# Kernel tuning notes

Measured on AMD Instinct MI355X. Metric: run time of the kernel, lower is better.

Reference implementation:

```python
import jax, jax.numpy as jnp
import numpy as np

B, T, A, H = 64, 512, 128, 512  # batch, timesteps, alphabet, hidden (m_size == H)


def setup_inputs() -> dict:
    key = jax.random.key(0)
    ks = jax.random.split(key, 8)
    s_ih = 1.0 / np.sqrt(H)
    return {
        "inputs": jax.random.normal(ks[0], (B, T, A), dtype=jnp.float32),
        # PyTorch LSTMCell params: gate order i, f, g, o
        "w_ih": jax.random.uniform(ks[1], (4 * H, A), jnp.float32, -s_ih, s_ih),
        "w_hh": jax.random.uniform(ks[2], (4 * H, H), jnp.float32, -s_ih, s_ih),
        "b_ih": jax.random.uniform(ks[3], (4 * H,), jnp.float32, -s_ih, s_ih),
        "b_hh": jax.random.uniform(ks[4], (4 * H,), jnp.float32, -s_ih, s_ih),
        # per-sample fast-weight matrix M (initialized to zeros in the module,
        # but trainable; use small random values so the bmm path is exercised)
        "M": jax.random.normal(ks[5], (B, H, H), dtype=jnp.float32) * 0.02,
        # hidden2out Linear
        "w_out": jax.random.uniform(ks[6], (A, H), jnp.float32, -s_ih, s_ih),
        "b_out": jax.random.uniform(ks[7], (A,), jnp.float32, -s_ih, s_ih),
        "h0": jnp.zeros((B, H), jnp.float32),
        "c0": jnp.zeros((B, H), jnp.float32),
    }


def reference(inputs, w_ih, w_hh, b_ih, b_hh, M, w_out, b_out, h0, c0):
    bias = b_ih + b_hh

    def step(carry, x_t):
        h, c = carry
        gates = x_t @ w_ih.T + h @ w_hh.T + bias  # [B, 4H]
        i, f, g, o = jnp.split(gates, 4, axis=1)
        i = jax.nn.sigmoid(i)
        f = jax.nn.sigmoid(f)
        g = jnp.tanh(g)
        o = jax.nn.sigmoid(o)
        c_new = f * c + i * g
        h_new = o * jnp.tanh(c_new)
        # fast-weight augmentation: h + M @ h (m_size == hidden_dim branch)
        h_aug = h_new + jnp.einsum('bij,bj->bi', M, h_new)
        out = h_aug @ w_out.T + b_out  # [B, A]
        # use_aug_in_recurrent=False: recurrent state stays un-augmented
        return (h_new, c_new), out

    xs = jnp.swapaxes(inputs, 0, 1)  # [T, B, A]
    _, outs = jax.lax.scan(step, (h0, c0), xs)  # outs: [T, B, A]
    return jnp.swapaxes(outs, 0, 1)  # [B, T, A]
```

## Files before the change

### kernel.cpp

```cpp
#include <hip/hip_runtime.h>
#include <hip/hip_bf16.h>

#define T_STEPS 512
#define B_SZ    64
#define A_SZ    128
#define H_SZ    512
#define NWG     256
#define THR     512

#define WEFF_SZ 4194304u
#define HBUF_SZ 65536u
#define BAR_U32 512u

#define W_F4    8192
#define ACT_F4  1280
#define LDSB    (4*(W_F4 + ACT_F4)*4 + 256)

__global__ __launch_bounds__(256) void weff_kernel(
    const float* __restrict__ M, const float* __restrict__ w_out,
    float* __restrict__ weff)
{
    __shared__ float wl[32*36];
    __shared__ float ml[32*68];
    const int blk = blockIdx.x;
    const int b   = blk >> 5;
    const int at  = (blk >> 3) & 3;
    const int jt  = blk & 7;
    const int tid = threadIdx.x;
    const int ap  = tid >> 4;
    const int jq  = tid & 15;
    float4 acc0 = {0.f,0.f,0.f,0.f};
    float4 acc1 = {0.f,0.f,0.f,0.f};

    for (int ik = 0; ik < 16; ++ik){
        {
            const int a = tid >> 3, i4 = tid & 7;
            const float4 v = *(const float4*)&w_out[(at*32 + a)*512 + ik*32 + i4*4];
            *(float4*)&wl[a*36 + i4*4] = v;
        }
        {
            const int i = tid >> 3, j8 = tid & 7;
            const float* src = &M[((size_t)b*512 + (size_t)(ik*32 + i))*512 + jt*64 + j8*8];
            const float4 v0 = *(const float4*)(src);
            const float4 v1 = *(const float4*)(src + 4);
            *(float4*)&ml[i*68 + j8*8]     = v0;
            *(float4*)&ml[i*68 + j8*8 + 4] = v1;
        }
        __syncthreads();
        #pragma unroll
        for (int i0 = 0; i0 < 32; i0 += 4){
            const float4 w0 = *(const float4*)&wl[(ap*2+0)*36 + i0];
            const float4 w1 = *(const float4*)&wl[(ap*2+1)*36 + i0];
            #pragma unroll
            for (int di = 0; di < 4; ++di){
                const float4 mv = *(const float4*)&ml[(i0+di)*68 + jq*4];
                const float wa = (di==0)?w0.x:(di==1)?w0.y:(di==2)?w0.z:w0.w;
                const float wb = (di==0)?w1.x:(di==1)?w1.y:(di==2)?w1.z:w1.w;
                acc0.x = fmaf(wa, mv.x, acc0.x); acc0.y = fmaf(wa, mv.y, acc0.y);
                acc0.z = fmaf(wa, mv.z, acc0.z); acc0.w = fmaf(wa, mv.w, acc0.w);
                acc1.x = fmaf(wb, mv.x, acc1.x); acc1.y = fmaf(wb, mv.y, acc1.y);
                acc1.z = fmaf(wb, mv.z, acc1.z); acc1.w = fmaf(wb, mv.w, acc1.w);
            }
        }
        __syncthreads();
    }
    const int ag = at*32 + ap*2;
    const int jg = jt*64 + jq*4;
    {
        const float4 id0 = *(const float4*)&w_out[(ag+0)*512 + jg];
        const float4 id1 = *(const float4*)&w_out[(ag+1)*512 + jg];
        float4 o0, o1;
        o0.x = acc0.x + id0.x; o0.y = acc0.y + id0.y; o0.z = acc0.z + id0.z; o0.w = acc0.w + id0.w;
        o1.x = acc1.x + id1.x; o1.y = acc1.y + id1.y; o1.z = acc1.z + id1.z; o1.w = acc1.w + id1.w;
        *(float4*)&weff[((size_t)b*128 + (ag+0))*512 + jg] = o0;
        *(float4*)&weff[((size_t)b*128 + (ag+1))*512 + jg] = o1;
    }
}

__global__ __launch_bounds__(THR) void rnn_kernel(
    const float* __restrict__ x,    const float* __restrict__ w_ih,
    const float* __restrict__ w_hh, const float* __restrict__ b_ih,
    const float* __restrict__ b_hh, const float* __restrict__ h0,
    const float* __restrict__ c0,   const float* __restrict__ b_out,
    const float* __restrict__ weff, float* __restrict__ hbuf,
    unsigned* __restrict__ barws,   float* __restrict__ out)
{
    extern __shared__ float lds[];
    float4* wlds4  = (float4*)lds;
    float4* act4   = ((float4*)lds) + W_F4;
    float*  bias_s = lds + 4*(W_F4 + ACT_F4);
    __shared__ unsigned role_s;

    const int tid = threadIdx.x;

    if (tid == 0){
        unsigned xcc;
        asm volatile("s_getreg_b32 %0, hwreg(20, 0, 32)" : "=s"(xcc));
        xcc &= 7u;
        const unsigned slot = __hip_atomic_fetch_add(&barws[xcc*64 + 2], 1u,
                                  __ATOMIC_RELAXED, __HIP_MEMORY_SCOPE_AGENT);
        role_s = (xcc << 5) | (slot & 31u);
    }
    __syncthreads();
    const int myx = (int)(role_s >> 5);
    const int s   = (int)(role_s & 31u);
    const int b0  = myx * 8;
    const int j0  = s * 16;

    unsigned* cnt = &barws[myx*64 + 0];
    unsigned* gen = &barws[myx*64 + 1];
    float* hbX = hbuf + myx * 8192;

    {
        const int r = tid >> 3, p = tid & 7;
        const int g = r & 3, jlr = r >> 2;
        const float4* src = (const float4*)&w_hh[(size_t)(g*H_SZ + j0 + jlr)*H_SZ];
        const int e = r & 7;
        #pragma unroll
        for (int m = 0; m < 16; ++m){
            const int sl = p*16 + m;
            wlds4[r*128 + (sl ^ e)] = src[sl];
        }
    }
    if (tid < 64){
        const int g = tid & 3, jlr = tid >> 2;
        const int grow = g*H_SZ + j0 + jlr;
        bias_s[tid] = b_ih[grow] + b_hh[grow];
    }

    const int jl  = tid >> 5;
    const int ks  = tid & 31;
    const int sb  = tid >> 6;
    const int l   = tid & 63;
    const int c_l = (tid >> 4) & 3;
    const int k_l = tid & 15;
    const int col = s*4 + c_l;
    const int eb  = sb & 7;

    float4 wihv[4];
    #pragma unroll
    for (int g = 0; g < 4; ++g)
        wihv[g] = *(const float4*)&w_ih[(size_t)(g*H_SZ + j0 + jl)*A_SZ + ks*4];

    float4 wef4[8];
    #pragma unroll
    for (int i8 = 0; i8 < 8; ++i8)
        wef4[i8] = *(const float4*)&weff[((size_t)(b0 + sb)*A_SZ + col)*H_SZ + (k_l + 16*i8)*4];
    const float bo = b_out[col];

    float cst[8];
    #pragma unroll
    for (int bb = 0; bb < 8; ++bb)
        cst[bb] = c0[(size_t)(b0 + bb)*H_SZ + j0 + jl];

    for (int t = 0; t <= T_STEPS; ++t){
        {
            const float* hprev = hbX + (((t+1)&1) ? 4096 : 0) + sb*H_SZ;
            const float4* h0r  = (const float4*)&h0[(size_t)(b0+sb)*H_SZ];
            const float4* xr   = (const float4*)&x[((size_t)(b0+sb)*T_STEPS + (t < T_STEPS ? t : 0))*A_SZ];
            auto stage_one = [&](int sl){
                float4 v;
                if (sl < 32){
                    if (t < T_STEPS){ v = xr[sl]; act4[sb*160 + (sl ^ eb)] = v; }
                } else if (t == 0){
                    v = h0r[sl - 32];
                    act4[sb*160 + (sl ^ eb)] = v;
                } else {
                    float* hp = (float*)(hprev + (sl - 32)*4);
                    v.x = __hip_atomic_load(hp+0, __ATOMIC_RELAXED, __HIP_MEMORY_SCOPE_AGENT);
                    v.y = __hip_atomic_load(hp+1, __ATOMIC_RELAXED, __HIP_MEMORY_SCOPE_AGENT);
                    v.z = __hip_atomic_load(hp+2, __ATOMIC_RELAXED, __HIP_MEMORY_SCOPE_AGENT);
                    v.w = __hip_atomic_load(hp+3, __ATOMIC_RELAXED, __HIP_MEMORY_SCOPE_AGENT);
                    act4[sb*160 + (sl ^ eb)] = v;
                }
            };
            stage_one(2*l);
            stage_one(2*l + 1);
            if (l < 32) stage_one(128 + l);
        }
        __syncthreads();

        if (t > 0){
            float p = 0.f;
            #pragma unroll
            for (int i8 = 0; i8 < 8; ++i8){
                const float4 av = act4[sb*160 + ((32 + k_l + 16*i8) ^ eb)];
                p = fmaf(wef4[i8].x, av.x, p);
                p = fmaf(wef4[i8].y, av.y, p);
                p = fmaf(wef4[i8].z, av.z, p);
                p = fmaf(wef4[i8].w, av.w, p);
            }
            p += __shfl_xor(p, 1); p += __shfl_xor(p, 2);
            p += __shfl_xor(p, 4); p += __shfl_xor(p, 8);
            if (k_l == 0)
                out[((size_t)(b0 + sb)*T_STEPS + (t-1))*A_SZ + col] = p + bo;
        }
        if (t == T_STEPS) break;

        float acc[4][8];
        #pragma unroll
        for (int g = 0; g < 4; ++g)
            #pragma unroll
            for (int bb = 0; bb < 8; ++bb) acc[g][bb] = 0.f;

        {
            float4 av[8];
            #pragma unroll
            for (int bb = 0; bb < 8; ++bb) av[bb] = act4[bb*160 + (ks ^ (bb&7))];
            #pragma unroll
            for (int g = 0; g < 4; ++g){
                #pragma unroll
                for (int bb = 0; bb < 8; ++bb){
                    acc[g][bb] = fmaf(wihv[g].x, av[bb].x, acc[g][bb]);
                    acc[g][bb] = fmaf(wihv[g].y, av[bb].y, acc[g][bb]);
                    acc[g][bb] = fmaf(wihv[g].z, av[bb].z, acc[g][bb]);
                    acc[g][bb] = fmaf(wihv[g].w, av[bb].w, acc[g][bb]);
                }
            }
        }
        #pragma unroll
        for (int m = 0; m < 4; ++m){
            const int hs = ks + 32*m;
            float4 wv[4];
            #pragma unroll
            for (int g = 0; g < 4; ++g){
                const int r = jl*4 + g;
                wv[g] = wlds4[r*128 + (hs ^ (r&7))];
            }
            float4 av[8];
            #pragma unroll
            for (int bb = 0; bb < 8; ++bb) av[bb] = act4[bb*160 + ((32 + hs) ^ (bb&7))];
            #pragma unroll
            for (int g = 0; g < 4; ++g)
                #pragma unroll
                for (int bb = 0; bb < 8; ++bb){
                    acc[g][bb] = fmaf(wv[g].x, av[bb].x, acc[g][bb]);
                    acc[g][bb] = fmaf(wv[g].y, av[bb].y, acc[g][bb]);
                    acc[g][bb] = fmaf(wv[g].z, av[bb].z, acc[g][bb]);
                    acc[g][bb] = fmaf(wv[g].w, av[bb].w, acc[g][bb]);
                }
        }
        #pragma unroll
        for (int g = 0; g < 4; ++g)
            #pragma unroll
            for (int bb = 0; bb < 8; ++bb){
                float v = acc[g][bb];
                v += __shfl_xor(v, 1);  v += __shfl_xor(v, 2);
                v += __shfl_xor(v, 4);  v += __shfl_xor(v, 8);
                v += __shfl_xor(v, 16);
                acc[g][bb] = v;
            }

        if (ks == 0){
            float* hc = hbX + ((t&1) ? 4096 : 0);
            #pragma unroll
            for (int bb = 0; bb < 8; ++bb){
                const float gi = acc[0][bb] + bias_s[jl*4 + 0];
                const float gf = acc[1][bb] + bias_s[jl*4 + 1];
                const float gg = acc[2][bb] + bias_s[jl*4 + 2];
                const float go = acc[3][bb] + bias_s[jl*4 + 3];
                const float si = 1.f / (1.f + __expf(-gi));
                const float sf = 1.f / (1.f + __expf(-gf));
                const float tg = tanhf(gg);
                const float so = 1.f / (1.f + __expf(-go));
                const float c  = sf * cst[bb] + si * tg;
                cst[bb] = c;
                const float h  = so * tanhf(c);
                __hip_atomic_store(&hc[bb*H_SZ + j0 + jl], h,
                                   __ATOMIC_RELAXED, __HIP_MEMORY_SCOPE_AGENT);
            }
        }
        __syncthreads();

        if (tid == 0){
            __atomic_signal_fence(__ATOMIC_SEQ_CST);
            const unsigned prev = __hip_atomic_fetch_add(cnt, 1u,
                                      __ATOMIC_RELAXED, __HIP_MEMORY_SCOPE_AGENT);
            if (prev + 1u == 32u*(unsigned)(t+1)){
                __hip_atomic_store(gen, (unsigned)(t+1),
                                   __ATOMIC_RELAXED, __HIP_MEMORY_SCOPE_AGENT);
            } else {
                while (__hip_atomic_load(gen, __ATOMIC_RELAXED,
                                         __HIP_MEMORY_SCOPE_AGENT) < (unsigned)(t+1))
                    __builtin_amdgcn_s_sleep(2);
            }
            __atomic_signal_fence(__ATOMIC_SEQ_CST);
        }
        __syncthreads();
    }
}

extern "C" void kernel_launch(void* const* d_in, const int* in_sizes, int n_in,
                              void* d_out, int out_size, void* d_ws, size_t ws_size,
                              hipStream_t stream)
{
    (void)in_sizes; (void)n_in; (void)out_size;
    const float* x     = (const float*)d_in[0];
    const float* w_ih  = (const float*)d_in[1];
    const float* w_hh  = (const float*)d_in[2];
    const float* b_ih  = (const float*)d_in[3];
    const float* b_hh  = (const float*)d_in[4];
    const float* M     = (const float*)d_in[5];
    const float* w_out = (const float*)d_in[6];
    const float* b_out = (const float*)d_in[7];
    const float* h0    = (const float*)d_in[8];
    const float* c0    = (const float*)d_in[9];
    float* out = (float*)d_out;

    const size_t need = (size_t)(WEFF_SZ + HBUF_SZ)*4 + BAR_U32*4;
    if (ws_size < need) return;

    float*    ws    = (float*)d_ws;
    float*    weff  = ws;
    float*    hbuf  = ws + WEFF_SZ;
    unsigned* barws = (unsigned*)(ws + WEFF_SZ + HBUF_SZ);

    hipMemsetAsync((void*)barws, 0, BAR_U32*4, stream);

    hipLaunchKernelGGL(weff_kernel, dim3(2048), dim3(256), 0, stream, M, w_out, weff);

    hipFuncSetAttribute((const void*)rnn_kernel,
                        hipFuncAttributeMaxDynamicSharedMemorySize, LDSB);

    void* args[] = {
        (void*)&x, (void*)&w_ih, (void*)&w_hh, (void*)&b_ih, (void*)&b_hh,
        (void*)&h0, (void*)&c0, (void*)&b_out, (void*)&weff, (void*)&hbuf,
        (void*)&barws, (void*)&out
    };
    hipLaunchCooperativeKernel((const void*)rnn_kernel, dim3(NWG), dim3(THR),
                               args, (unsigned)LDSB, stream);
}
```

Baseline: 12.90 ms.

## Replace counter barrier with per-block flags, register-resident weights, DPP reductions

```diff
diff --git a/kernel.cpp b/kernel.cpp
--- a/kernel.cpp
+++ b/kernel.cpp
@@ -10,11 +10,8 @@
 
 #define WEFF_SZ 4194304u
 #define HBUF_SZ 65536u
-#define BAR_U32 512u
-
-#define W_F4    8192
-#define ACT_F4  1280
-#define LDSB    (4*(W_F4 + ACT_F4)*4 + 256)
+#define BAR_U32 2048u
+#define LDSB    98304
 
 __global__ __launch_bounds__(256) void weff_kernel(
     const float* __restrict__ M, const float* __restrict__ w_out,
@@ -77,7 +74,29 @@
     }
 }
 
-__global__ __launch_bounds__(THR) void rnn_kernel(
+template<int CTRL>
+__device__ __forceinline__ float dppadd(float v){
+    const int o = __builtin_amdgcn_mov_dpp(__float_as_int(v), CTRL, 0xF, 0xF, true);
+    return v + __int_as_float(o);
+}
+__device__ __forceinline__ float red16(float v){
+    v = dppadd<0xB1>(v); v = dppadd<0x4E>(v);
+    v = dppadd<0x141>(v); v = dppadd<0x140>(v);
+    return v;
+}
+__device__ __forceinline__ float red32(float v){
+    v = red16(v);
+    v += __int_as_float(__builtin_amdgcn_ds_swizzle(__float_as_int(v), 0x401F));
+    return v;
+}
+__device__ __forceinline__ float sigm(float x){ return 1.f / (1.f + __expf(-x)); }
+__device__ __forceinline__ float tanh_fast(float x){
+    const float xc = fminf(fmaxf(x, -9.f), 9.f);
+    const float e  = __expf(2.f * xc);
+    return (e - 1.f) * (1.f / (e + 1.f));
+}
+
+__global__ __launch_bounds__(THR, 2) void rnn_kernel(
     const float* __restrict__ x,    const float* __restrict__ w_ih,
     const float* __restrict__ w_hh, const float* __restrict__ b_ih,
     const float* __restrict__ b_hh, const float* __restrict__ h0,
@@ -86,9 +105,7 @@
     unsigned* __restrict__ barws,   float* __restrict__ out)
 {
     extern __shared__ float lds[];
-    float4* wlds4  = (float4*)lds;
-    float4* act4   = ((float4*)lds) + W_F4;
-    float*  bias_s = lds + 4*(W_F4 + ACT_F4);
+    float4* act = (float4*)lds;
     __shared__ unsigned role_s;
 
     const int tid = threadIdx.x;
@@ -97,7 +114,7 @@
         unsigned xcc;
         asm volatile("s_getreg_b32 %0, hwreg(20, 0, 32)" : "=s"(xcc));
         xcc &= 7u;
-        const unsigned slot = __hip_atomic_fetch_add(&barws[xcc*64 + 2], 1u,
+        const unsigned slot = __hip_atomic_fetch_add(&barws[xcc*256 + 0], 1u,
                                   __ATOMIC_RELAXED, __HIP_MEMORY_SCOPE_AGENT);
         role_s = (xcc << 5) | (slot & 31u);
     }
@@ -107,26 +124,8 @@
     const int b0  = myx * 8;
     const int j0  = s * 16;
 
-    unsigned* cnt = &barws[myx*64 + 0];
-    unsigned* gen = &barws[myx*64 + 1];
-    float* hbX = hbuf + myx * 8192;
-
-    {
-        const int r = tid >> 3, p = tid & 7;
-        const int g = r & 3, jlr = r >> 2;
-        const float4* src = (const float4*)&w_hh[(size_t)(g*H_SZ + j0 + jlr)*H_SZ];
-        const int e = r & 7;
-        #pragma unroll
-        for (int m = 0; m < 16; ++m){
-            const int sl = p*16 + m;
-            wlds4[r*128 + (sl ^ e)] = src[sl];
-        }
-    }
-    if (tid < 64){
-        const int g = tid & 3, jlr = tid >> 2;
-        const int grow = g*H_SZ + j0 + jlr;
-        bias_s[tid] = b_ih[grow] + b_hh[grow];
-    }
+    unsigned* flg  = barws + myx*256 + 32;
+    float*    hbX  = hbuf + myx * 8192;
 
     const int jl  = tid >> 5;
     const int ks  = tid & 31;
@@ -135,158 +134,158 @@
     const int c_l = (tid >> 4) & 3;
     const int k_l = tid & 15;
     const int col = s*4 + c_l;
-    const int eb  = sb & 7;
-
+
+    float4 whh[4][4];
+    #pragma unroll
+    for (int g = 0; g < 4; ++g)
+        #pragma unroll
+        for (int m = 0; m < 4; ++m)
+            whh[g][m] = *(const float4*)&w_hh[(size_t)(g*H_SZ + j0 + jl)*H_SZ + (ks + 32*m)*4];
     float4 wihv[4];
     #pragma unroll
     for (int g = 0; g < 4; ++g)
         wihv[g] = *(const float4*)&w_ih[(size_t)(g*H_SZ + j0 + jl)*A_SZ + ks*4];
-
+    float bg[4];
+    #pragma unroll
+    for (int g = 0; g < 4; ++g){
+        const int grow = g*H_SZ + j0 + jl;
+        bg[g] = b_ih[grow] + b_hh[grow];
+    }
     float4 wef4[8];
     #pragma unroll
     for (int i8 = 0; i8 < 8; ++i8)
         wef4[i8] = *(const float4*)&weff[((size_t)(b0 + sb)*A_SZ + col)*H_SZ + (k_l + 16*i8)*4];
     const float bo = b_out[col];
-
-    float cst[8];
+    float cst = c0[(size_t)(b0 + (ks & 7))*H_SZ + j0 + jl];
+
+    float4 xv[8];
     #pragma unroll
     for (int bb = 0; bb < 8; ++bb)
-        cst[bb] = c0[(size_t)(b0 + bb)*H_SZ + j0 + jl];
+        xv[bb] = *(const float4*)&x[((size_t)(b0+bb)*T_STEPS + 0)*A_SZ + ks*4];
 
     for (int t = 0; t <= T_STEPS; ++t){
         {
-            const float* hprev = hbX + (((t+1)&1) ? 4096 : 0) + sb*H_SZ;
-            const float4* h0r  = (const float4*)&h0[(size_t)(b0+sb)*H_SZ];
-            const float4* xr   = (const float4*)&x[((size_t)(b0+sb)*T_STEPS + (t < T_STEPS ? t : 0))*A_SZ];
-            auto stage_one = [&](int sl){
-                float4 v;
-                if (sl < 32){
-                    if (t < T_STEPS){ v = xr[sl]; act4[sb*160 + (sl ^ eb)] = v; }
-                } else if (t == 0){
-                    v = h0r[sl - 32];
-                    act4[sb*160 + (sl ^ eb)] = v;
-                } else {
-                    float* hp = (float*)(hprev + (sl - 32)*4);
-                    v.x = __hip_atomic_load(hp+0, __ATOMIC_RELAXED, __HIP_MEMORY_SCOPE_AGENT);
-                    v.y = __hip_atomic_load(hp+1, __ATOMIC_RELAXED, __HIP_MEMORY_SCOPE_AGENT);
-                    v.z = __hip_atomic_load(hp+2, __ATOMIC_RELAXED, __HIP_MEMORY_SCOPE_AGENT);
-                    v.w = __hip_atomic_load(hp+3, __ATOMIC_RELAXED, __HIP_MEMORY_SCOPE_AGENT);
-                    act4[sb*160 + (sl ^ eb)] = v;
+            const int bb = sb;
+            if (t > 0){
+                unsigned* f1 = flg + ((l >> 2)       ) * 4;
+                unsigned* f2 = flg + (16 + (l >> 2)  ) * 4;
+                while (__hip_atomic_load(f1, __ATOMIC_RELAXED, __HIP_MEMORY_SCOPE_AGENT)
+                       < (unsigned)t) __builtin_amdgcn_s_sleep(1);
+                while (__hip_atomic_load(f2, __ATOMIC_RELAXED, __HIP_MEMORY_SCOPE_AGENT)
+                       < (unsigned)t) __builtin_amdgcn_s_sleep(1);
+            }
+            const float4* hb = (t == 0)
+                ? ((const float4*)h0)  + (size_t)(b0 + bb)*128
+                : ((const float4*)hbX) + (((t+1)&1) ? 1024 : 0) + bb*128;
+            const float4* p1 = hb + l;
+            const float4* p2 = hb + l + 64;
+            float4 v1, v2;
+            asm volatile("global_load_dwordx4 %0, %2, off sc0\n\t"
+                         "global_load_dwordx4 %1, %3, off sc0\n\t"
+                         "s_waitcnt vmcnt(0)"
+                         : "=&v"(v1), "=&v"(v2) : "v"(p1), "v"(p2) : "memory");
+            act[bb*128 + l]      = v1;
+            act[bb*128 + l + 64] = v2;
+        }
+        __syncthreads();
+
+        if (t < T_STEPS){
+            float acc[4][8];
+            #pragma unroll
+            for (int g = 0; g < 4; ++g)
+                #pragma unroll
+                for (int bb = 0; bb < 8; ++bb) acc[g][bb] = 0.f;
+
+            #pragma unroll
+            for (int bb = 0; bb < 8; ++bb){
+                const float4 av = xv[bb];
+                #pragma unroll
+                for (int g = 0; g < 4; ++g){
+                    acc[g][bb] = fmaf(wihv[g].x, av.x, acc[g][bb]);
+                    acc[g][bb] = fmaf(wihv[g].y, av.y, acc[g][bb]);
+                    acc[g][bb] = fmaf(wihv[g].z, av.z, acc[g][bb]);
+                    acc[g][bb] = fmaf(wihv[g].w, av.w, acc[g][bb]);
                 }
-            };
-            stage_one(2*l);
-            stage_one(2*l + 1);
-            if (l < 32) stage_one(128 + l);
-        }
-        __syncthreads();
+            }
+            #pragma unroll
+            for (int m = 0; m < 4; ++m){
+                float4 av[8];
+                #pragma unroll
+                for (int bb = 0; bb < 8; ++bb) av[bb] = act[bb*128 + ks + 32*m];
+                #pragma unroll
+                for (int g = 0; g < 4; ++g){
+                    const float4 wv = whh[g][m];
+                    #pragma unroll
+                    for (int bb = 0; bb < 8; ++bb){
+                        acc[g][bb] = fmaf(wv.x, av[bb].x, acc[g][bb]);
+                        acc[g][bb] = fmaf(wv.y, av[bb].y, acc[g][bb]);
+                        acc[g][bb] = fmaf(wv.z, av[bb].z, acc[g][bb]);
+                        acc[g][bb] = fmaf(wv.w, av[bb].w, acc[g][bb]);
+                    }
+                }
+            }
+            #pragma unroll
+            for (int g = 0; g < 4; ++g)
+                #pragma unroll
+                for (int bb = 0; bb < 8; ++bb)
+                    acc[g][bb] = red32(acc[g][bb]);
+
+            float ga[4];
+            const bool q0 = ks & 1, q1 = ks & 2, q2 = ks & 4;
+            #pragma unroll
+            for (int g = 0; g < 4; ++g){
+                const float a01 = q0 ? acc[g][1] : acc[g][0];
+                const float a23 = q0 ? acc[g][3] : acc[g][2];
+                const float a45 = q0 ? acc[g][5] : acc[g][4];
+                const float a67 = q0 ? acc[g][7] : acc[g][6];
+                const float a03 = q1 ? a23 : a01;
+                const float a47 = q1 ? a67 : a45;
+                ga[g] = q2 ? a47 : a03;
+            }
+            if (ks < 8){
+                const float gi = ga[0] + bg[0];
+                const float gf = ga[1] + bg[1];
+                const float gg = ga[2] + bg[2];
+                const float go = ga[3] + bg[3];
+                const float si = sigm(gi);
+                const float sf = sigm(gf);
+                const float tg = tanh_fast(gg);
+                const float so = sigm(go);
+                const float c  = sf * cst + si * tg;
+                cst = c;
+                const float h  = so * tanh_fast(c);
+                float* hw = hbX + ((t&1) ? 4096 : 0);
+                hw[(size_t)ks*H_SZ + j0 + jl] = h;
+            }
+        }
 
         if (t > 0){
             float p = 0.f;
             #pragma unroll
             for (int i8 = 0; i8 < 8; ++i8){
-                const float4 av = act4[sb*160 + ((32 + k_l + 16*i8) ^ eb)];
+                const float4 av = act[sb*128 + k_l + 16*i8];
                 p = fmaf(wef4[i8].x, av.x, p);
                 p = fmaf(wef4[i8].y, av.y, p);
                 p = fmaf(wef4[i8].z, av.z, p);
                 p = fmaf(wef4[i8].w, av.w, p);
             }
-            p += __shfl_xor(p, 1); p += __shfl_xor(p, 2);
-            p += __shfl_xor(p, 4); p += __shfl_xor(p, 8);
+            p = red16(p);
             if (k_l == 0)
                 out[((size_t)(b0 + sb)*T_STEPS + (t-1))*A_SZ + col] = p + bo;
         }
         if (t == T_STEPS) break;
 
-        float acc[4][8];
-        #pragma unroll
-        for (int g = 0; g < 4; ++g)
-            #pragma unroll
-            for (int bb = 0; bb < 8; ++bb) acc[g][bb] = 0.f;
-
-        {
-            float4 av[8];
-            #pragma unroll
-            for (int bb = 0; bb < 8; ++bb) av[bb] = act4[bb*160 + (ks ^ (bb&7))];
-            #pragma unroll
-            for (int g = 0; g < 4; ++g){
-                #pragma unroll
-                for (int bb = 0; bb < 8; ++bb){
-                    acc[g][bb] = fmaf(wihv[g].x, av[bb].x, acc[g][bb]);
-                    acc[g][bb] = fmaf(wihv[g].y, av[bb].y, acc[g][bb]);
-                    acc[g][bb] = fmaf(wihv[g].z, av[bb].z, acc[g][bb]);
-                    acc[g][bb] = fmaf(wihv[g].w, av[bb].w, acc[g][bb]);
-                }
-            }
-        }
-        #pragma unroll
-        for (int m = 0; m < 4; ++m){
-            const int hs = ks + 32*m;
-            float4 wv[4];
-            #pragma unroll
-            for (int g = 0; g < 4; ++g){
-                const int r = jl*4 + g;
-                wv[g] = wlds4[r*128 + (hs ^ (r&7))];
-            }
-            float4 av[8];
-            #pragma unroll
-            for (int bb = 0; bb < 8; ++bb) av[bb] = act4[bb*160 + ((32 + hs) ^ (bb&7))];
-            #pragma unroll
-            for (int g = 0; g < 4; ++g)
-                #pragma unroll
-                for (int bb = 0; bb < 8; ++bb){
-                    acc[g][bb] = fmaf(wv[g].x, av[bb].x, acc[g][bb]);
-                    acc[g][bb] = fmaf(wv[g].y, av[bb].y, acc[g][bb]);
-                    acc[g][bb] = fmaf(wv[g].z, av[bb].z, acc[g][bb]);
-                    acc[g][bb] = fmaf(wv[g].w, av[bb].w, acc[g][bb]);
-                }
-        }
-        #pragma unroll
-        for (int g = 0; g < 4; ++g)
-            #pragma unroll
-            for (int bb = 0; bb < 8; ++bb){
-                float v = acc[g][bb];
-                v += __shfl_xor(v, 1);  v += __shfl_xor(v, 2);
-                v += __shfl_xor(v, 4);  v += __shfl_xor(v, 8);
-                v += __shfl_xor(v, 16);
-                acc[g][bb] = v;
-            }
-
-        if (ks == 0){
-            float* hc = hbX + ((t&1) ? 4096 : 0);
-            #pragma unroll
-            for (int bb = 0; bb < 8; ++bb){
-                const float gi = acc[0][bb] + bias_s[jl*4 + 0];
-                const float gf = acc[1][bb] + bias_s[jl*4 + 1];
-                const float gg = acc[2][bb] + bias_s[jl*4 + 2];
-                const float go = acc[3][bb] + bias_s[jl*4 + 3];
-                const float si = 1.f / (1.f + __expf(-gi));
-                const float sf = 1.f / (1.f + __expf(-gf));
-                const float tg = tanhf(gg);
-                const float so = 1.f / (1.f + __expf(-go));
-                const float c  = sf * cst[bb] + si * tg;
-                cst[bb] = c;
-                const float h  = so * tanhf(c);
-                __hip_atomic_store(&hc[bb*H_SZ + j0 + jl], h,
-                                   __ATOMIC_RELAXED, __HIP_MEMORY_SCOPE_AGENT);
-            }
-        }
         __syncthreads();
 
-        if (tid == 0){
-            __atomic_signal_fence(__ATOMIC_SEQ_CST);
-            const unsigned prev = __hip_atomic_fetch_add(cnt, 1u,
-                                      __ATOMIC_RELAXED, __HIP_MEMORY_SCOPE_AGENT);
-            if (prev + 1u == 32u*(unsigned)(t+1)){
-                __hip_atomic_store(gen, (unsigned)(t+1),
-                                   __ATOMIC_RELAXED, __HIP_MEMORY_SCOPE_AGENT);
-            } else {
-                while (__hip_atomic_load(gen, __ATOMIC_RELAXED,
-                                         __HIP_MEMORY_SCOPE_AGENT) < (unsigned)(t+1))
-                    __builtin_amdgcn_s_sleep(2);
-            }
-            __atomic_signal_fence(__ATOMIC_SEQ_CST);
-        }
-        __syncthreads();
+        if (tid == 0)
+            __hip_atomic_store(flg + s*4, (unsigned)(t+1),
+                               __ATOMIC_RELAXED, __HIP_MEMORY_SCOPE_AGENT);
+
+        if (t + 1 < T_STEPS){
+            #pragma unroll
+            for (int bb = 0; bb < 8; ++bb)
+                xv[bb] = *(const float4*)&x[((size_t)(b0+bb)*T_STEPS + (t+1))*A_SZ + ks*4];
+        }
     }
 }
 
```

Measured after the change: 12.08 ms. -6.3%, faster.
